# Performance work log

Measured on AMD Instinct MI355X. Metric: run time of the kernel, lower is better.

## Reference

```python
import jax, jax.numpy as jnp
import numpy as np

D_MODEL = 1024
H = 16
D_K = D_MODEL // H
B, S = 4, 2048


def setup_inputs() -> dict:
    key = jax.random.key(0)
    ks = jax.random.split(key, 12)
    s = 1.0 / np.sqrt(D_MODEL)
    inp = {
        "q": jax.random.normal(ks[0], (B, S, D_MODEL), jnp.float32),
        "k": jax.random.normal(ks[1], (B, S, D_MODEL), jnp.float32),
        "v": jax.random.normal(ks[2], (B, S, D_MODEL), jnp.float32),
        "mask": jax.random.randint(ks[3], (1, 1, S, S), 0, 2, jnp.int32),
        # torch nn.Linear convention: weight [out, in], y = x @ W.T + b
        "w_q": jax.random.uniform(ks[4], (D_MODEL, D_MODEL), jnp.float32, -s, s),
        "b_q": jax.random.uniform(ks[5], (D_MODEL,), jnp.float32, -s, s),
        "w_k": jax.random.uniform(ks[6], (D_MODEL, D_MODEL), jnp.float32, -s, s),
        "b_k": jax.random.uniform(ks[7], (D_MODEL,), jnp.float32, -s, s),
        "w_v": jax.random.uniform(ks[8], (D_MODEL, D_MODEL), jnp.float32, -s, s),
        "b_v": jax.random.uniform(ks[9], (D_MODEL,), jnp.float32, -s, s),
        "w_o": jax.random.uniform(ks[10], (D_MODEL, D_MODEL), jnp.float32, -s, s),
        "b_o": jax.random.uniform(ks[11], (D_MODEL,), jnp.float32, -s, s),
    }
    return inp


def _split_heads(x):
    b, s, _ = x.shape
    return x.reshape(b, s, H, D_K).transpose(0, 2, 1, 3)  # [B,H,S,Dk]


def reference(q, k, v, mask, w_q, b_q, w_k, b_k, w_v, b_v, w_o, b_o):
    query = _split_heads(q @ w_q.T + b_q)
    key = _split_heads(k @ w_k.T + b_k)
    value = _split_heads(v @ w_v.T + b_v)
    scores = jnp.einsum("bhqd,bhkd->bhqk", query, key) / jnp.sqrt(
        jnp.asarray(D_K, query.dtype))
    scores = jnp.where(mask == 0, jnp.asarray(-1e9, scores.dtype), scores)
    attn = jax.nn.softmax(scores, axis=-1)  # dropout p=0 (eval) -> identity
    x = jnp.einsum("bhqk,bhkd->bhqd", attn, value)
    x = x.transpose(0, 2, 1, 3).reshape(q.shape[0], -1, H * D_K)
    return x @ w_o.T + b_o
```

## Files before the change

### kernel.cpp

```cpp
#include <hip/hip_runtime.h>

typedef __bf16 bf16_t;
typedef __bf16 bf16x4 __attribute__((ext_vector_type(4)));
typedef __bf16 bf16x8 __attribute__((ext_vector_type(8)));
typedef float f32x4 __attribute__((ext_vector_type(4)));
typedef float f32x16 __attribute__((ext_vector_type(16)));
typedef unsigned int uint;
typedef uint uint4v __attribute__((ext_vector_type(4)));

#define CSCALE 0.18033688011112042f

static __device__ __forceinline__ bf16_t f2bf(float f) {
  unsigned u = __builtin_bit_cast(unsigned, f);
  u = (u + 0x7fff + ((u >> 16) & 1)) >> 16;
  unsigned short h = (unsigned short)u;
  return __builtin_bit_cast(bf16_t, h);
}
static __device__ __forceinline__ uint cvt_pk(float a, float b) {
  uint r;
  asm("v_cvt_pk_bf16_f32 %0, %1, %2" : "=v"(r) : "v"(a), "v"(b));
  return r;
}

#define GLD_LDS(g, l) \
  __builtin_amdgcn_global_load_lds((const __attribute__((address_space(1))) void*)(g), \
                                   (__attribute__((address_space(3))) void*)(l), 16, 0, 0)

__global__ void cvt4_f2b(const float* __restrict__ a, const float* __restrict__ b,
                         const float* __restrict__ c, const float* __restrict__ d,
                         bf16_t* __restrict__ oa, bf16_t* __restrict__ ob,
                         bf16_t* __restrict__ oc, bf16_t* __restrict__ od) {
  int i = blockIdx.x * 256 + threadIdx.x;
  const float* src = a;
  bf16_t* dst = oa;
  int w = i >> 18;
  i &= 262143;
  if (w == 1) { src = b; dst = ob; }
  else if (w == 2) { src = c; dst = oc; }
  else if (w == 3) { src = d; dst = od; }
  const float4 f = reinterpret_cast<const float4*>(src)[i];
  bf16x4 o;
  o[0] = f2bf(f.x); o[1] = f2bf(f.y); o[2] = f2bf(f.z); o[3] = f2bf(f.w);
  reinterpret_cast<bf16x4*>(dst)[i] = o;
}

__global__ void mask_bits_k(const int* __restrict__ m, uint* __restrict__ out) {
  int i = blockIdx.x * 256 + threadIdx.x;
  int q = i & 2047, t = i >> 11;
  const int* mrow = m + (size_t)q * 2048 + t * 32;
  uint bits = 0;
#pragma unroll
  for (int j = 0; j < 16; ++j) {
    int r0 = (j & 3) + 8 * (j >> 2);
    bits |= (mrow[r0] ? 1u : 0u) << j;
    bits |= (mrow[r0 + 4] ? 1u : 0u) << (16 + j);
  }
  out[(size_t)t * 2048 + q] = bits;
}

__global__ __launch_bounds__(256, 2) void qkv_gemm(
    const float* __restrict__ qA, const float* __restrict__ kA, const float* __restrict__ vA,
    const bf16_t* __restrict__ wq, const bf16_t* __restrict__ wk, const bf16_t* __restrict__ wv,
    const float* __restrict__ bq, const float* __restrict__ bk, const float* __restrict__ bv,
    bf16_t* __restrict__ Qp, bf16_t* __restrict__ Kp, bf16_t* __restrict__ Vt) {
  constexpr int K = 1024, N = 1024;
  __shared__ __align__(16) float Asf[128 * 32];
  __shared__ __align__(16) bf16_t Bs[128 * 32];
  const int z = blockIdx.z;
  const float* A = (z == 0) ? qA : (z == 1) ? kA : vA;
  const bf16_t* W = (z == 0) ? wq : (z == 1) ? wk : wv;
  const float* bias = (z == 0) ? bq : (z == 1) ? bk : bv;

  const int tid = threadIdx.x;
  const int lane = tid & 63;
  const int wv_ = tid >> 6;
  const int wm = (wv_ >> 1) * 64, wn = (wv_ & 1) * 64;
  const int l15 = lane & 15, lhi = lane >> 4;
  const int bm = blockIdx.x, bn = blockIdx.y;

  const int rA = tid >> 3;
  const float* gA = A + (size_t)(bm * 128 + rA) * K + ((tid & 7) ^ (rA & 7)) * 4;
  const int rB = tid >> 2;
  const bf16_t* gB = W + (size_t)(bn * 128 + rB) * K + ((tid & 3) ^ (rB & 3)) * 8;

  f32x4 acc[4][4] = {};
  for (int k0 = 0; k0 < K; k0 += 32) {
    __syncthreads();
#pragma unroll
    for (int c2 = 0; c2 < 4; ++c2)
      GLD_LDS(gA + (size_t)c2 * 32 * K + k0, (char*)Asf + c2 * 4096 + wv_ * 1024);
#pragma unroll
    for (int c2 = 0; c2 < 2; ++c2)
      GLD_LDS(gB + (size_t)c2 * 64 * K + k0, (char*)Bs + c2 * 4096 + wv_ * 1024);
    __syncthreads();
    bf16x8 af[4], bfv[4];
#pragma unroll
    for (int i = 0; i < 4; ++i) {
      int arow = wm + i * 16 + l15;
      f32x4 a0 = *reinterpret_cast<const f32x4*>(
          (const char*)Asf + arow * 128 + (((2 * lhi) ^ (arow & 7)) * 16));
      f32x4 a1 = *reinterpret_cast<const f32x4*>(
          (const char*)Asf + arow * 128 + (((2 * lhi + 1) ^ (arow & 7)) * 16));
      uint4v ua;
      ua[0] = cvt_pk(a0[0], a0[1]);
      ua[1] = cvt_pk(a0[2], a0[3]);
      ua[2] = cvt_pk(a1[0], a1[1]);
      ua[3] = cvt_pk(a1[2], a1[3]);
      af[i] = __builtin_bit_cast(bf16x8, ua);
    }
#pragma unroll
    for (int j = 0; j < 4; ++j) {
      int brow = wn + j * 16 + l15;
      bfv[j] = *reinterpret_cast<const bf16x8*>(
          (const char*)Bs + brow * 64 + ((lhi ^ (brow & 3)) * 16));
    }
#pragma unroll
    for (int i = 0; i < 4; ++i)
#pragma unroll
      for (int j = 0; j < 4; ++j)
        acc[i][j] = __builtin_amdgcn_mfma_f32_16x16x32_bf16(af[i], bfv[j], acc[i][j], 0, 0, 0);
  }
#pragma unroll
  for (int i = 0; i < 4; ++i) {
#pragma unroll
    for (int j = 0; j < 4; ++j) {
      int n = bn * 128 + wn + j * 16 + l15;
      float bv2 = bias[n];
#pragma unroll
      for (int r = 0; r < 4; ++r) {
        int m = bm * 128 + wm + i * 16 + lhi * 4 + r;
        float val = acc[i][j][r] + bv2;
        if (z == 0) {
          Qp[(size_t)m * N + n] = f2bf(val * CSCALE);
        } else if (z == 1) {
          Kp[(size_t)m * N + n] = f2bf(val);
        } else {
          int b = m >> 11, s = m & 2047;
          Vt[((size_t)b * 1024 + n) * 2048 + s] = f2bf(val);
        }
      }
    }
  }
}

__global__ __launch_bounds__(256, 2) void gemm_o(
    const bf16_t* __restrict__ A, const bf16_t* __restrict__ Bw,
    const float* __restrict__ bias, float* __restrict__ Cout) {
  constexpr int K = 1024, N = 1024;
  __shared__ __align__(16) bf16_t As[128 * 32];
  __shared__ __align__(16) bf16_t Bs[128 * 32];
  const int tid = threadIdx.x;
  const int lane = tid & 63;
  const int wv_ = tid >> 6;
  const int wm = (wv_ >> 1) * 64, wn = (wv_ & 1) * 64;
  const int l15 = lane & 15, lhi = lane >> 4;
  const int bm = blockIdx.x, bn = blockIdx.y;
  const int rB = tid >> 2;
  const bf16_t* ga = A + (size_t)(bm * 128 + rB) * K + ((tid & 3) ^ (rB & 3)) * 8;
  const bf16_t* gb = Bw + (size_t)(bn * 128 + rB) * K + ((tid & 3) ^ (rB & 3)) * 8;
  f32x4 acc[4][4] = {};
  for (int k0 = 0; k0 < K; k0 += 32) {
    __syncthreads();
#pragma unroll
    for (int c2 = 0; c2 < 2; ++c2) {
      GLD_LDS(ga + (size_t)c2 * 64 * K + k0, (char*)As + c2 * 4096 + wv_ * 1024);
      GLD_LDS(gb + (size_t)c2 * 64 * K + k0, (char*)Bs + c2 * 4096 + wv_ * 1024);
    }
    __syncthreads();
    bf16x8 af[4], bfv[4];
#pragma unroll
    for (int i = 0; i < 4; ++i) {
      int arow = wm + i * 16 + l15;
      af[i] = *reinterpret_cast<const bf16x8*>(
          (const char*)As + arow * 64 + ((lhi ^ (arow & 3)) * 16));
    }
#pragma unroll
    for (int j = 0; j < 4; ++j) {
      int brow = wn + j * 16 + l15;
      bfv[j] = *reinterpret_cast<const bf16x8*>(
          (const char*)Bs + brow * 64 + ((lhi ^ (brow & 3)) * 16));
    }
#pragma unroll
    for (int i = 0; i < 4; ++i)
#pragma unroll
      for (int j = 0; j < 4; ++j)
        acc[i][j] = __builtin_amdgcn_mfma_f32_16x16x32_bf16(af[i], bfv[j], acc[i][j], 0, 0, 0);
  }
#pragma unroll
  for (int i = 0; i < 4; ++i)
#pragma unroll
    for (int j = 0; j < 4; ++j) {
      int n = bn * 128 + wn + j * 16 + l15;
      float bv2 = bias[n];
#pragma unroll
      for (int r = 0; r < 4; ++r) {
        int m = bm * 128 + wm + i * 16 + lhi * 4 + r;
        Cout[(size_t)m * N + n] = acc[i][j][r] + bv2;
      }
    }
}

static __device__ __forceinline__ f32x16 qk_tile(const bf16_t* Kbuf, const bf16x8 qf[4],
                                                 int l31, int h) {
  f32x16 s = {};
  __builtin_amdgcn_s_setprio(1);
#pragma unroll
  for (int c = 0; c < 4; ++c) {
    bf16x8 kf = *reinterpret_cast<const bf16x8*>(Kbuf + l31 * 64 + ((h + 2 * c) ^ (l31 & 7)) * 8);
    s = __builtin_amdgcn_mfma_f32_32x32x16_bf16(kf, qf[c], s, 0, 0, 0);
  }
  __builtin_amdgcn_s_setprio(0);
  return s;
}

static __device__ __forceinline__ void softmax_tile(
    const f32x16& sv, uint mb, int h, f32x16& o0, f32x16& o1,
    float& mrun, float& lsum, bf16x8& pa0, bf16x8& pa1) {
  const uint mbh = mb >> (h << 4);
  float a0 = fmaxf(fmaxf(sv[0], sv[1]), sv[2]);
  float a1 = fmaxf(fmaxf(sv[3], sv[4]), sv[5]);
  float a2 = fmaxf(fmaxf(sv[6], sv[7]), sv[8]);
  float a3 = fmaxf(fmaxf(sv[9], sv[10]), sv[11]);
  float a4 = fmaxf(fmaxf(sv[12], sv[13]), sv[14]);
  float b0 = fmaxf(fmaxf(a0, a1), a2);
  float mt = fmaxf(fmaxf(b0, fmaxf(a3, a4)), sv[15]);
  if (!__all(mt - mrun <= 8.0f)) {
    float mtf = fmaxf(mt, __shfl_xor(mt, 32));
    float mnew = fmaxf(mrun, mtf);
    float alpha = __builtin_amdgcn_exp2f(mrun - mnew);
    lsum *= alpha;
#pragma unroll
    for (int r = 0; r < 16; ++r) {
      float ar = __shfl(alpha, (r & 3) + 8 * (r >> 2) + 4 * h);
      o0[r] *= ar; o1[r] *= ar;
    }
    mrun = mnew;
  }
  float p[16];
#pragma unroll
  for (int r = 0; r < 16; ++r) {
    float pv = __builtin_amdgcn_exp2f(sv[r] - mrun);
    uint smask = (uint)__builtin_amdgcn_sbfe((int)mbh, r, 1);
    p[r] = __builtin_bit_cast(float, __builtin_bit_cast(uint, pv) & smask);
  }
  float t0 = p[0] + p[1], t1 = p[2] + p[3], t2 = p[4] + p[5], t3 = p[6] + p[7];
  float t4 = p[8] + p[9], t5 = p[10] + p[11], t6 = p[12] + p[13], t7 = p[14] + p[15];
  t0 += t1; t2 += t3; t4 += t5; t6 += t7;
  lsum += (t0 + t2) + (t4 + t6);
  uint dw[8];
#pragma unroll
  for (int i = 0; i < 8; ++i) dw[i] = cvt_pk(p[2 * i], p[2 * i + 1]);
  uint e0 = (uint)__shfl_xor((int)(h ? dw[0] : dw[2]), 32);
  uint e1 = (uint)__shfl_xor((int)(h ? dw[1] : dw[3]), 32);
  uint e2 = (uint)__shfl_xor((int)(h ? dw[4] : dw[6]), 32);
  uint e3 = (uint)__shfl_xor((int)(h ? dw[5] : dw[7]), 32);
  uint4v ua0 = {h ? e0 : dw[0], h ? e1 : dw[1], h ? dw[2] : e0, h ? dw[3] : e1};
  uint4v ua1 = {h ? e2 : dw[4], h ? e3 : dw[5], h ? dw[6] : e2, h ? dw[7] : e3};
  pa0 = __builtin_bit_cast(bf16x8, ua0);
  pa1 = __builtin_bit_cast(bf16x8, ua1);
}

static __device__ __forceinline__ void pv_tile(const bf16_t* Vbuf, bf16x8 pa0, bf16x8 pa1,
                                               int l31, int h, f32x16& o0, f32x16& o1) {
  const int sw = l31 & 3;
  bf16x8 v00 = *reinterpret_cast<const bf16x8*>(Vbuf + l31 * 32 + ((h ^ sw) * 8));
  bf16x8 v01 = *reinterpret_cast<const bf16x8*>(Vbuf + l31 * 32 + (((2 + h) ^ sw) * 8));
  bf16x8 v10 = *reinterpret_cast<const bf16x8*>(Vbuf + (32 + l31) * 32 + ((h ^ sw) * 8));
  bf16x8 v11 = *reinterpret_cast<const bf16x8*>(Vbuf + (32 + l31) * 32 + (((2 + h) ^ sw) * 8));
  __builtin_amdgcn_s_setprio(1);
  o0 = __builtin_amdgcn_mfma_f32_32x32x16_bf16(pa0, v00, o0, 0, 0, 0);
  o0 = __builtin_amdgcn_mfma_f32_32x32x16_bf16(pa1, v01, o0, 0, 0, 0);
  o1 = __builtin_amdgcn_mfma_f32_32x32x16_bf16(pa0, v10, o1, 0, 0, 0);
  o1 = __builtin_amdgcn_mfma_f32_32x32x16_bf16(pa1, v11, o1, 0, 0, 0);
  __builtin_amdgcn_s_setprio(0);
}

__global__ __launch_bounds__(256, 4) void attn_kernel(
    const bf16_t* __restrict__ Qp, const bf16_t* __restrict__ Kp,
    const bf16_t* __restrict__ Vt, const uint* __restrict__ maskbits,
    bf16_t* __restrict__ Xb) {
  constexpr int S = 2048, D = 1024;
  __shared__ __align__(16) bf16_t Ks[2][32][64];
  __shared__ __align__(16) bf16_t Vs[2][64][32];
  const int tid = threadIdx.x;
  const int wv_ = tid >> 6, lane = tid & 63;
  const int l31 = lane & 31, h = lane >> 5;
  const int blk = blockIdx.x;
  const int bh = blk & 63, qt4 = blk >> 6;
  const int b = bh >> 4, hd = bh & 15;
  const int q0 = qt4 * 128 + wv_ * 32;

  const int rK = tid >> 3;
  const bf16_t* gK = Kp + ((size_t)b * S + rK) * D + hd * 64 + ((tid & 7) ^ (rK & 7)) * 8;
  const int rV = tid >> 2;
  const bf16_t* gV = Vt + ((size_t)b * 1024 + hd * 64 + rV) * (size_t)S + ((tid & 3) ^ (rV & 3)) * 8;
  char* ldsK0 = (char*)&Ks[0][0][0] + wv_ * 1024;
  char* ldsK1 = (char*)&Ks[1][0][0] + wv_ * 1024;
  char* ldsV0 = (char*)&Vs[0][0][0] + wv_ * 1024;
  char* ldsV1 = (char*)&Vs[1][0][0] + wv_ * 1024;

  const bf16_t* qbase = Qp + (size_t)(b * S + q0 + l31) * D + hd * 64 + h * 8;
  bf16x8 qf[4];
#pragma unroll
  for (int c = 0; c < 4; ++c)
    qf[c] = *reinterpret_cast<const bf16x8*>(qbase + 16 * c);

  const uint* mbase = maskbits + q0 + l31;

  f32x16 o0 = {}, o1 = {};
  float mrun = 0.f, lsum = 0.f;
  bf16x8 pa0, pa1;

  GLD_LDS(gK, ldsK0);
  GLD_LDS(gK + (size_t)32 * D, ldsK1);
  GLD_LDS(gV, ldsV0);
  uint mb0 = mbase[0];
  __syncthreads();
  {
    f32x16 s = qk_tile(&Ks[0][0][0], qf, l31, h);
    softmax_tile(s, mb0, h, o0, o1, mrun, lsum, pa0, pa1);
  }

  auto body = [&](int j, char* ldsK_st, char* ldsV_st, const bf16_t* Kq,
                  const bf16_t* Vp, bool stageK) {
    if (stageK) GLD_LDS(gK + (size_t)(j + 2) * 32 * D, ldsK_st);
    GLD_LDS(gV + (size_t)(j + 1) * 32, ldsV_st);
    uint mbn = mbase[(size_t)(j + 1) * 2048];
    f32x16 s = qk_tile(Kq, qf, l31, h);
    pv_tile(Vp, pa0, pa1, l31, h, o0, o1);
    softmax_tile(s, mbn, h, o0, o1, mrun, lsum, pa0, pa1);
    __syncthreads();
  };

#pragma unroll 1
  for (int jj = 0; jj < 31; ++jj) {
    const int j = 2 * jj;
    body(j,     ldsK0, ldsV1, &Ks[1][0][0], &Vs[0][0][0], true);
    body(j + 1, ldsK1, ldsV0, &Ks[0][0][0], &Vs[1][0][0], true);
  }
  body(62, ldsK0, ldsV1, &Ks[1][0][0], &Vs[0][0][0], false);
  pv_tile(&Vs[1][0][0], pa0, pa1, l31, h, o0, o1);

  lsum += __shfl_xor(lsum, 32);
  float linv = __builtin_amdgcn_rcpf(lsum);
  bf16_t* xrow = Xb + (size_t)(b * S + q0) * D + hd * 64 + l31;
#pragma unroll
  for (int r = 0; r < 16; ++r) {
    int qrow = (r & 3) + 8 * (r >> 2) + 4 * h;
    float lr = __shfl(linv, qrow);
    xrow[(size_t)qrow * D] = f2bf(o0[r] * lr);
    xrow[(size_t)qrow * D + 32] = f2bf(o1[r] * lr);
  }
}

extern "C" void kernel_launch(void* const* d_in, const int* in_sizes, int n_in,
                              void* d_out, int out_size, void* d_ws, size_t ws_size,
                              hipStream_t stream) {
  const float* q = (const float*)d_in[0];
  const float* k = (const float*)d_in[1];
  const float* v = (const float*)d_in[2];
  const int* mask = (const int*)d_in[3];
  const float* w_q = (const float*)d_in[4];
  const float* b_q = (const float*)d_in[5];
  const float* w_k = (const float*)d_in[6];
  const float* b_k = (const float*)d_in[7];
  const float* w_v = (const float*)d_in[8];
  const float* b_v = (const float*)d_in[9];
  const float* w_o = (const float*)d_in[10];
  const float* b_o = (const float*)d_in[11];

  char* ws = (char*)d_ws;
  const size_t SZ = (size_t)8192 * 1024 * 2;
  bf16_t* Qp = (bf16_t*)(ws + 0 * SZ);
  bf16_t* Kp = (bf16_t*)(ws + 1 * SZ);
  bf16_t* Vt = (bf16_t*)(ws + 2 * SZ);
  bf16_t* Xb = (bf16_t*)(ws + 3 * SZ);
  uint* maskB = (uint*)(ws + 4 * SZ);
  bf16_t* wqb = (bf16_t*)(ws + 4 * SZ + 8388608);
  bf16_t* wkb = wqb + 1048576;
  bf16_t* wvb = wkb + 1048576;
  bf16_t* wob = wvb + 1048576;

  cvt4_f2b<<<4096, 256, 0, stream>>>(w_q, w_k, w_v, w_o, wqb, wkb, wvb, wob);
  mask_bits_k<<<512, 256, 0, stream>>>(mask, maskB);

  dim3 g3(64, 8, 3);
  qkv_gemm<<<g3, 256, 0, stream>>>(q, k, v, wqb, wkb, wvb, b_q, b_k, b_v, Qp, Kp, Vt);
  attn_kernel<<<1024, 256, 0, stream>>>(Qp, Kp, Vt, maskB, Xb);
  gemm_o<<<dim3(64, 8), 256, 0, stream>>>(Xb, wob, b_o, (float*)d_out);
}
```

Measured before the change: 253.4 us.

## Double-buffer LDS tiles in QKV and output projection GEMMs

```diff
diff --git a/kernel.cpp b/kernel.cpp
--- a/kernel.cpp
+++ b/kernel.cpp
@@ -64,8 +64,8 @@
     const float* __restrict__ bq, const float* __restrict__ bk, const float* __restrict__ bv,
     bf16_t* __restrict__ Qp, bf16_t* __restrict__ Kp, bf16_t* __restrict__ Vt) {
   constexpr int K = 1024, N = 1024;
-  __shared__ __align__(16) float Asf[128 * 32];
-  __shared__ __align__(16) bf16_t Bs[128 * 32];
+  __shared__ __align__(16) float Asf[2][128 * 32];
+  __shared__ __align__(16) bf16_t Bs[2][128 * 32];
   const int z = blockIdx.z;
   const float* A = (z == 0) ? qA : (z == 1) ? kA : vA;
   const bf16_t* W = (z == 0) ? wq : (z == 1) ? wk : wv;
@@ -84,23 +84,24 @@
   const bf16_t* gB = W + (size_t)(bn * 128 + rB) * K + ((tid & 3) ^ (rB & 3)) * 8;
 
   f32x4 acc[4][4] = {};
-  for (int k0 = 0; k0 < K; k0 += 32) {
-    __syncthreads();
+
+  auto STAGE = [&](int t, int buf) {
 #pragma unroll
     for (int c2 = 0; c2 < 4; ++c2)
-      GLD_LDS(gA + (size_t)c2 * 32 * K + k0, (char*)Asf + c2 * 4096 + wv_ * 1024);
+      GLD_LDS(gA + (size_t)c2 * 32 * K + t * 32, (char*)&Asf[buf][0] + c2 * 4096 + wv_ * 1024);
 #pragma unroll
     for (int c2 = 0; c2 < 2; ++c2)
-      GLD_LDS(gB + (size_t)c2 * 64 * K + k0, (char*)Bs + c2 * 4096 + wv_ * 1024);
-    __syncthreads();
+      GLD_LDS(gB + (size_t)c2 * 64 * K + t * 32, (char*)&Bs[buf][0] + c2 * 4096 + wv_ * 1024);
+  };
+  auto COMPUTE = [&](int buf) {
     bf16x8 af[4], bfv[4];
 #pragma unroll
     for (int i = 0; i < 4; ++i) {
       int arow = wm + i * 16 + l15;
       f32x4 a0 = *reinterpret_cast<const f32x4*>(
-          (const char*)Asf + arow * 128 + (((2 * lhi) ^ (arow & 7)) * 16));
+          (const char*)&Asf[buf][0] + arow * 128 + (((2 * lhi) ^ (arow & 7)) * 16));
       f32x4 a1 = *reinterpret_cast<const f32x4*>(
-          (const char*)Asf + arow * 128 + (((2 * lhi + 1) ^ (arow & 7)) * 16));
+          (const char*)&Asf[buf][0] + arow * 128 + (((2 * lhi + 1) ^ (arow & 7)) * 16));
       uint4v ua;
       ua[0] = cvt_pk(a0[0], a0[1]);
       ua[1] = cvt_pk(a0[2], a0[3]);
@@ -112,14 +113,25 @@
     for (int j = 0; j < 4; ++j) {
       int brow = wn + j * 16 + l15;
       bfv[j] = *reinterpret_cast<const bf16x8*>(
-          (const char*)Bs + brow * 64 + ((lhi ^ (brow & 3)) * 16));
+          (const char*)&Bs[buf][0] + brow * 64 + ((lhi ^ (brow & 3)) * 16));
     }
 #pragma unroll
     for (int i = 0; i < 4; ++i)
 #pragma unroll
       for (int j = 0; j < 4; ++j)
         acc[i][j] = __builtin_amdgcn_mfma_f32_16x16x32_bf16(af[i], bfv[j], acc[i][j], 0, 0, 0);
-  }
+  };
+
+  STAGE(0, 0);
+  __syncthreads();
+#pragma unroll 1
+  for (int jj = 0; jj < 15; ++jj) {
+    STAGE(2 * jj + 1, 1); COMPUTE(0); __syncthreads();
+    STAGE(2 * jj + 2, 0); COMPUTE(1); __syncthreads();
+  }
+  STAGE(31, 1); COMPUTE(0); __syncthreads();
+  COMPUTE(1);
+
 #pragma unroll
   for (int i = 0; i < 4; ++i) {
 #pragma unroll
@@ -147,8 +159,8 @@
     const bf16_t* __restrict__ A, const bf16_t* __restrict__ Bw,
     const float* __restrict__ bias, float* __restrict__ Cout) {
   constexpr int K = 1024, N = 1024;
-  __shared__ __align__(16) bf16_t As[128 * 32];
-  __shared__ __align__(16) bf16_t Bs[128 * 32];
+  __shared__ __align__(16) bf16_t As[2][128 * 32];
+  __shared__ __align__(16) bf16_t Bs[2][128 * 32];
   const int tid = threadIdx.x;
   const int lane = tid & 63;
   const int wv_ = tid >> 6;
@@ -159,33 +171,45 @@
   const bf16_t* ga = A + (size_t)(bm * 128 + rB) * K + ((tid & 3) ^ (rB & 3)) * 8;
   const bf16_t* gb = Bw + (size_t)(bn * 128 + rB) * K + ((tid & 3) ^ (rB & 3)) * 8;
   f32x4 acc[4][4] = {};
-  for (int k0 = 0; k0 < K; k0 += 32) {
-    __syncthreads();
+
+  auto STAGE = [&](int t, int buf) {
 #pragma unroll
     for (int c2 = 0; c2 < 2; ++c2) {
-      GLD_LDS(ga + (size_t)c2 * 64 * K + k0, (char*)As + c2 * 4096 + wv_ * 1024);
-      GLD_LDS(gb + (size_t)c2 * 64 * K + k0, (char*)Bs + c2 * 4096 + wv_ * 1024);
-    }
-    __syncthreads();
+      GLD_LDS(ga + (size_t)c2 * 64 * K + t * 32, (char*)&As[buf][0] + c2 * 4096 + wv_ * 1024);
+      GLD_LDS(gb + (size_t)c2 * 64 * K + t * 32, (char*)&Bs[buf][0] + c2 * 4096 + wv_ * 1024);
+    }
+  };
+  auto COMPUTE = [&](int buf) {
     bf16x8 af[4], bfv[4];
 #pragma unroll
     for (int i = 0; i < 4; ++i) {
       int arow = wm + i * 16 + l15;
       af[i] = *reinterpret_cast<const bf16x8*>(
-          (const char*)As + arow * 64 + ((lhi ^ (arow & 3)) * 16));
+          (const char*)&As[buf][0] + arow * 64 + ((lhi ^ (arow & 3)) * 16));
     }
 #pragma unroll
     for (int j = 0; j < 4; ++j) {
       int brow = wn + j * 16 + l15;
       bfv[j] = *reinterpret_cast<const bf16x8*>(
-          (const char*)Bs + brow * 64 + ((lhi ^ (brow & 3)) * 16));
+          (const char*)&Bs[buf][0] + brow * 64 + ((lhi ^ (brow & 3)) * 16));
     }
 #pragma unroll
     for (int i = 0; i < 4; ++i)
 #pragma unroll
       for (int j = 0; j < 4; ++j)
         acc[i][j] = __builtin_amdgcn_mfma_f32_16x16x32_bf16(af[i], bfv[j], acc[i][j], 0, 0, 0);
-  }
+  };
+
+  STAGE(0, 0);
+  __syncthreads();
+#pragma unroll 1
+  for (int jj = 0; jj < 15; ++jj) {
+    STAGE(2 * jj + 1, 1); COMPUTE(0); __syncthreads();
+    STAGE(2 * jj + 2, 0); COMPUTE(1); __syncthreads();
+  }
+  STAGE(31, 1); COMPUTE(0); __syncthreads();
+  COMPUTE(1);
+
 #pragma unroll
   for (int i = 0; i < 4; ++i)
 #pragma unroll
```

Result: no change. 250.7 us (-1.1%).
